# Kernel tuning notes

Measured on AMD Instinct MI355X. Metric: run time of the kernel, lower is better.

The kernel has to match this reference:

```python
import jax, jax.numpy as jnp
import numpy as np

B, T, K, H, HID, OUT = 128, 128, 8, 3, 256, 2
LOG_STD_MIN, LOG_STD_MAX = -20.0, 2.0


def setup_inputs() -> dict:
    key = jax.random.key(0)
    ks = jax.random.split(key, 12)
    def lin(k, fan_in, fan_out, scale=0.05):
        return jax.random.normal(k, (fan_in, fan_out), dtype=jnp.float32) * scale
    return {
        "state": jax.random.normal(ks[0], (B, T, K), dtype=jnp.float32),
        "noise": jax.random.normal(ks[1], (B, T, OUT), dtype=jnp.float32),
        "Wq": lin(ks[2], K, H * K),
        "Wk": lin(ks[3], K, H * K),
        "Wv": lin(ks[4], K, H * K),
        "W1": lin(ks[5], H * K + K, HID),
        "b1": jnp.zeros((HID,), jnp.float32),
        "W2": lin(ks[6], HID, HID),
        "b2": jnp.zeros((HID,), jnp.float32),
        "Wmu": jax.random.uniform(ks[7], (HID, OUT), jnp.float32, -0.003, 0.003),
        "bmu": jax.random.uniform(ks[8], (OUT,), jnp.float32, -0.003, 0.003),
        "Wls": jax.random.uniform(ks[9], (HID, OUT), jnp.float32, -0.003, 0.003),
        "bls": jax.random.uniform(ks[10], (OUT,), jnp.float32, -0.003, 0.003),
    }


def reference(state, noise, Wq, Wk, Wv, W1, b1, W2, b2, Wmu, bmu, Wls, bls):
    b, t, k = state.shape
    h = H
    # off-diagonal gather indices: idx[i, m] = m if m < i else m + 1  (j != i, ascending)
    cols = jnp.arange(t - 1)
    idx = cols[None, :] + (cols[None, :] >= jnp.arange(t)[:, None]).astype(jnp.int32)  # [t, t-1]
    # rel_state[b, i, m] = state[b, idx[i, m]] - state[b, i]   -> [b, t, t-1, k]
    rel = state[:, idx, :] - state[:, :, None, :]
    # per-head projections (no bias)
    q = (state @ Wq).reshape(b, t, h, k)                      # [b, t, h, k]
    keys = (rel @ Wk).reshape(b, t, t - 1, h, k)              # [b, t, t-1, h, k]
    vals = (rel @ Wv).reshape(b, t, t - 1, h, k)
    # each query attends over its own t-1 relative keys
    scores = jnp.einsum("bthk,btmhk->bhtm", q, keys) / jnp.sqrt(jnp.float32(k))
    w = jax.nn.softmax(scores, axis=-1)                       # [b, h, t, t-1]
    x = jnp.einsum("bhtm,btmhk->bthk", w, vals).reshape(b, t, h * k)
    x = jnp.concatenate([x, state], axis=-1)                  # [b, t, h*k + k]
    x = jax.nn.relu(x @ W1 + b1)
    x = jax.nn.relu(x @ W2 + b2)
    mu = jnp.tanh(x @ Wmu + bmu)
    log_std = jnp.tanh(x @ Wls + bls)
    log_std = LOG_STD_MIN + 0.5 * (LOG_STD_MAX - LOG_STD_MIN) * (log_std + 1.0)
    std = jnp.exp(log_std)
    z = mu + std * noise                                      # rsample
    action = jnp.tanh(z)
    half_log_2pi = jnp.float32(0.5 * np.log(2.0 * np.pi))
    normal_lp = -0.5 * noise * noise - log_std - half_log_2pi
    log_prob = normal_lp - jnp.log(1.0 - action * action + 1e-7)
    log_prob = jnp.sum(log_prob, axis=-1, keepdims=True)
    return action, log_prob
```

## Files before the change

kernel.cpp:

```cpp
#include <hip/hip_runtime.h>
#include <math.h>

namespace {
constexpr int B_  = 128;
constexpr int T_  = 128;
constexpr int K_  = 8;
constexpr int H_  = 3;
constexpr int HK_ = 24;
constexpr int HID_ = 256;
constexpr int OUT_ = 2;
}

typedef __attribute__((ext_vector_type(8))) short bf16x8;
typedef __attribute__((ext_vector_type(4))) float f32x4;

__device__ inline unsigned short f2bf(float x) {
    unsigned int u = __float_as_uint(x);
    u += 0x7FFFu + ((u >> 16) & 1u);
    return (unsigned short)(u >> 16);
}
__device__ inline float bflo(unsigned int u) { return __uint_as_float(u << 16); }
__device__ inline float bfhi(unsigned int u) { return __uint_as_float(u & 0xFFFF0000u); }

template <int CTRL>
__device__ inline float dpp_add(float v) {
    int t = __builtin_amdgcn_update_dpp(0, __float_as_int(v), CTRL, 0xF, 0xF, true);
    return v + __int_as_float(t);
}
__device__ inline float red8(float v) {
    v = dpp_add<0xB1>(v);
    v = dpp_add<0x4E>(v);
    return dpp_add<0x141>(v);
}
__device__ inline float red16(float v) {
    return dpp_add<0x140>(red8(v));
}

__global__ __launch_bounds__(256) void prep_kernel(
    const float* __restrict__ W1, const float* __restrict__ W2,
    unsigned short* __restrict__ w1t, unsigned short* __restrict__ w2t)
{
    const int n = threadIdx.x;
    unsigned short tmp[8];
    if (blockIdx.x < 32) {
        const int k0 = blockIdx.x * 8;
        #pragma unroll
        for (int i = 0; i < 8; ++i) tmp[i] = f2bf(W2[(size_t)(k0+i)*HID_ + n]);
        *(bf16x8*)(w2t + (size_t)n*256 + k0) = *(const bf16x8*)tmp;
    } else {
        const int k0 = (blockIdx.x - 32) * 8;
        #pragma unroll
        for (int i = 0; i < 8; ++i) tmp[i] = f2bf(W1[(size_t)(k0+i)*HID_ + n]);
        *(bf16x8*)(w1t + (size_t)n*32 + k0) = *(const bf16x8*)tmp;
    }
}

__global__ __launch_bounds__(256) void fused_actor_kernel(
    const float* __restrict__ state,
    const float* __restrict__ noise,
    const float* __restrict__ Wq, const float* __restrict__ Wk,
    const float* __restrict__ Wv,
    const unsigned short* __restrict__ w1t, const float* __restrict__ b1,
    const unsigned short* __restrict__ w2t, const float* __restrict__ b2,
    const float* __restrict__ Wmu, const float* __restrict__ bmu,
    const float* __restrict__ Wls, const float* __restrict__ bls,
    float* __restrict__ out)
{
    __shared__ float wq_s[K_*HK_], wk_s[K_*HK_], wv_s[K_*HK_];
    __shared__ alignas(16) unsigned short Kb[H_][T_][8];
    __shared__ alignas(16) unsigned short Vb[H_][T_][8];
    __shared__ alignas(16) float Qs[32][HK_];
    __shared__ alignas(16) unsigned short a0b[32][40];
    __shared__ alignas(16) unsigned short x1s[32][264];
    __shared__ alignas(16) float hp[4][32][4];

    const int tid  = threadIdx.x;
    const int b    = blockIdx.x >> 2;
    const int iq   = blockIdx.x & 3;
    const int i0   = iq * 32;
    const int w    = tid >> 6;
    const int lane = tid & 63;
    const float* sb = state + (size_t)b*T_*K_;

    if (tid < K_*HK_) { wq_s[tid]=Wq[tid]; wk_s[tid]=Wk[tid]; wv_s[tid]=Wv[tid]; }
    __syncthreads();

    {
        const int j = tid >> 1, p = tid & 1;
        const float4 s0 = *(const float4*)(sb + j*8);
        const float4 s1 = *(const float4*)(sb + j*8 + 4);
        const float sv[8] = {s0.x,s0.y,s0.z,s0.w,s1.x,s1.y,s1.z,s1.w};
        const float* ws = p ? wv_s : wk_s;
        #pragma unroll
        for (int h = 0; h < H_; ++h) {
            unsigned short pk[8];
            #pragma unroll
            for (int k = 0; k < 8; ++k) {
                const int col = h*8 + k;
                float a = 0.f;
                #pragma unroll
                for (int m = 0; m < K_; ++m) a = fmaf(sv[m], ws[m*HK_+col], a);
                pk[k] = f2bf(a);
            }
            unsigned short* dst = p ? &Vb[h][j][0] : &Kb[h][j][0];
            *(bf16x8*)dst = *(const bf16x8*)pk;
        }
        if (p == 0 && j >= i0 && j < i0 + 32) {
            unsigned short sb16[8];
            #pragma unroll
            for (int k = 0; k < 8; ++k) sb16[k] = f2bf(sv[k]);
            *(bf16x8*)&a0b[j - i0][HK_] = *(const bf16x8*)sb16;
        }
    }
    {
        const int il = tid >> 3;
        const int c0 = (tid & 7) * 3;
        const float4 s0 = *(const float4*)(sb + (i0+il)*8);
        const float4 s1 = *(const float4*)(sb + (i0+il)*8 + 4);
        const float sv[8] = {s0.x,s0.y,s0.z,s0.w,s1.x,s1.y,s1.z,s1.w};
        #pragma unroll
        for (int cc = 0; cc < 3; ++cc) {
            const int col = c0 + cc;
            float aq = 0.f;
            #pragma unroll
            for (int m = 0; m < K_; ++m) aq = fmaf(sv[m], wq_s[m*HK_+col], aq);
            Qs[il][col] = aq * 0.35355339059327373f;
        }
    }
    __syncthreads();

    {
        const int i_sub = lane >> 3, jg = lane & 7;
        #pragma unroll
        for (int p = 0; p < 3; ++p) {
            const int pair = w*3 + p;
            const int h  = pair >> 2;
            const int ig = pair & 3;
            const int il = ig*8 + i_sub;
            const int iglob = i0 + il;
            const float4 q0 = *(const float4*)&Qs[il][h*8];
            const float4 q1 = *(const float4*)&Qs[il][h*8+4];
            float l = 0.f;
            float acc[8] = {0.f,0.f,0.f,0.f,0.f,0.f,0.f,0.f};
            #pragma unroll 4
            for (int t = 0; t < 16; ++t) {
                const int j = t*8 + jg;
                const int4 kk = *(const int4*)&Kb[h][j][0];
                float s;
                s = q0.x * bflo(kk.x) + q0.y * bfhi(kk.x)
                  + q0.z * bflo(kk.y) + q0.w * bfhi(kk.y)
                  + q1.x * bflo(kk.z) + q1.y * bfhi(kk.z)
                  + q1.z * bflo(kk.w) + q1.w * bfhi(kk.w);
                const float e = (j == iglob) ? 0.f : __expf(s);
                l += e;
                const int4 vv = *(const int4*)&Vb[h][j][0];
                acc[0] = fmaf(e, bflo(vv.x), acc[0]);
                acc[1] = fmaf(e, bfhi(vv.x), acc[1]);
                acc[2] = fmaf(e, bflo(vv.y), acc[2]);
                acc[3] = fmaf(e, bfhi(vv.y), acc[3]);
                acc[4] = fmaf(e, bflo(vv.z), acc[4]);
                acc[5] = fmaf(e, bfhi(vv.z), acc[5]);
                acc[6] = fmaf(e, bflo(vv.w), acc[6]);
                acc[7] = fmaf(e, bfhi(vv.w), acc[7]);
            }
            l = red8(l);
            #pragma unroll
            for (int k = 0; k < 8; ++k) acc[k] = red8(acc[k]);
            if (jg == 0) {
                const float rl = 1.f / l;
                const int4 vi = *(const int4*)&Vb[h][iglob][0];
                const float vs[8] = { bflo(vi.x), bfhi(vi.x), bflo(vi.y), bfhi(vi.y),
                                      bflo(vi.z), bfhi(vi.z), bflo(vi.w), bfhi(vi.w) };
                unsigned int r01 = (unsigned int)f2bf(acc[0]*rl - vs[0])
                                 | ((unsigned int)f2bf(acc[1]*rl - vs[1]) << 16);
                unsigned int r23 = (unsigned int)f2bf(acc[2]*rl - vs[2])
                                 | ((unsigned int)f2bf(acc[3]*rl - vs[3]) << 16);
                unsigned int r45 = (unsigned int)f2bf(acc[4]*rl - vs[4])
                                 | ((unsigned int)f2bf(acc[5]*rl - vs[5]) << 16);
                unsigned int r67 = (unsigned int)f2bf(acc[6]*rl - vs[6])
                                 | ((unsigned int)f2bf(acc[7]*rl - vs[7]) << 16);
                int4 rr; rr.x = r01; rr.y = r23; rr.z = r45; rr.w = r67;
                *(int4*)&a0b[il][h*8] = rr;
            }
        }
    }
    __syncthreads();

    const int lq = (tid >> 4) & 3;
    const int ln = tid & 15;

    {
        const bf16x8 a0 = *(const bf16x8*)&a0b[ln][lq*8];
        const bf16x8 a1 = *(const bf16x8*)&a0b[16+ln][lq*8];
        #pragma unroll
        for (int nt = 0; nt < 4; ++nt) {
            const int n0 = (w*4 + nt)*16;
            const bf16x8 bf = *(const bf16x8*)(w1t + (size_t)(n0+ln)*32 + lq*8);
            const float bias = b1[n0+ln];
            f32x4 c = {bias, bias, bias, bias};
            f32x4 d0 = __builtin_amdgcn_mfma_f32_16x16x32_bf16(a0, bf, c, 0, 0, 0);
            f32x4 d1 = __builtin_amdgcn_mfma_f32_16x16x32_bf16(a1, bf, c, 0, 0, 0);
            #pragma unroll
            for (int r = 0; r < 4; ++r) {
                x1s[lq*4 + r][n0+ln]      = f2bf(fmaxf(d0[r], 0.f));
                x1s[16 + lq*4 + r][n0+ln] = f2bf(fmaxf(d1[r], 0.f));
            }
        }
    }
    __syncthreads();

    f32x4 acc2[2][4];
    #pragma unroll
    for (int nt = 0; nt < 4; ++nt) {
        const float bias = b2[(w*4+nt)*16 + ln];
        f32x4 c = {bias, bias, bias, bias};
        acc2[0][nt] = c; acc2[1][nt] = c;
    }
    #pragma unroll 2
    for (int ks = 0; ks < 8; ++ks) {
        const int k0 = ks*32;
        const bf16x8 a0 = *(const bf16x8*)&x1s[ln][k0 + lq*8];
        const bf16x8 a1 = *(const bf16x8*)&x1s[16+ln][k0 + lq*8];
        #pragma unroll
        for (int nt = 0; nt < 4; ++nt) {
            const bf16x8 bf = *(const bf16x8*)(w2t + (size_t)((w*4+nt)*16+ln)*256 + k0 + lq*8);
            acc2[0][nt] = __builtin_amdgcn_mfma_f32_16x16x32_bf16(a0, bf, acc2[0][nt], 0,0,0);
            acc2[1][nt] = __builtin_amdgcn_mfma_f32_16x16x32_bf16(a1, bf, acc2[1][nt], 0,0,0);
        }
    }

    {
        float p[2][4][4];
        #pragma unroll
        for (int mt = 0; mt < 2; ++mt)
            #pragma unroll
            for (int r = 0; r < 4; ++r)
                #pragma unroll
                for (int o = 0; o < 4; ++o) p[mt][r][o] = 0.f;
        #pragma unroll
        for (int nt = 0; nt < 4; ++nt) {
            const int n = (w*4+nt)*16 + ln;
            const float2 wm = *(const float2*)(Wmu + n*OUT_);
            const float2 wl = *(const float2*)(Wls + n*OUT_);
            #pragma unroll
            for (int mt = 0; mt < 2; ++mt) {
                #pragma unroll
                for (int r = 0; r < 4; ++r) {
                    const float x2 = fmaxf(acc2[mt][nt][r], 0.f);
                    p[mt][r][0] = fmaf(x2, wm.x, p[mt][r][0]);
                    p[mt][r][1] = fmaf(x2, wm.y, p[mt][r][1]);
                    p[mt][r][2] = fmaf(x2, wl.x, p[mt][r][2]);
                    p[mt][r][3] = fmaf(x2, wl.y, p[mt][r][3]);
                }
            }
        }
        #pragma unroll
        for (int mt = 0; mt < 2; ++mt)
            #pragma unroll
            for (int r = 0; r < 4; ++r)
                #pragma unroll
                for (int o = 0; o < 4; ++o)
                    p[mt][r][o] = red16(p[mt][r][o]);
        if (ln == 0) {
            #pragma unroll
            for (int mt = 0; mt < 2; ++mt)
                #pragma unroll
                for (int r = 0; r < 4; ++r) {
                    f32x4 pv = {p[mt][r][0], p[mt][r][1], p[mt][r][2], p[mt][r][3]};
                    *(f32x4*)&hp[w][mt*16 + lq*4 + r][0] = pv;
                }
        }
    }
    __syncthreads();

    if (tid < 32) {
        const int r = tid;
        const int grow = b*T_ + i0 + r;
        float pre[4];
        #pragma unroll
        for (int o = 0; o < 4; ++o)
            pre[o] = hp[0][r][o] + hp[1][r][o] + hp[2][r][o] + hp[3][r][o];
        float lp = 0.f;
        #pragma unroll
        for (int o = 0; o < OUT_; ++o) {
            float mu  = tanhf(pre[o]   + bmu[o]);
            float lsp = tanhf(pre[2+o] + bls[o]);
            float log_std = -20.f + 11.f * (lsp + 1.f);
            float sd = __expf(log_std);
            float n  = noise[(size_t)grow*OUT_ + o];
            float z  = fmaf(sd, n, mu);
            float a  = tanhf(z);
            out[(size_t)grow*OUT_ + o] = a;
            lp += -0.5f*n*n - log_std - 0.91893853320467274f
                  - logf(1.f - a*a + 1e-7f);
        }
        out[(size_t)B_*T_*OUT_ + grow] = lp;
    }
}

extern "C" void kernel_launch(void* const* d_in, const int* in_sizes, int n_in,
                              void* d_out, int out_size, void* d_ws, size_t ws_size,
                              hipStream_t stream)
{
    const float* state = (const float*)d_in[0];
    const float* noise = (const float*)d_in[1];
    const float* Wq  = (const float*)d_in[2];
    const float* Wk  = (const float*)d_in[3];
    const float* Wv  = (const float*)d_in[4];
    const float* W1  = (const float*)d_in[5];
    const float* b1  = (const float*)d_in[6];
    const float* W2  = (const float*)d_in[7];
    const float* b2  = (const float*)d_in[8];
    const float* Wmu = (const float*)d_in[9];
    const float* bmu = (const float*)d_in[10];
    const float* Wls = (const float*)d_in[11];
    const float* bls = (const float*)d_in[12];
    float* out = (float*)d_out;

    unsigned short* w1t = (unsigned short*)d_ws;
    unsigned short* w2t = w1t + 8192;

    prep_kernel<<<dim3(36), dim3(256), 0, stream>>>(W1, W2, w1t, w2t);
    fused_actor_kernel<<<dim3(B_*4), dim3(256), 0, stream>>>(
        state, noise, Wq, Wk, Wv, w1t, b1, w2t, b2, Wmu, bmu, Wls, bls, out);
}
```

Before: 101.9 us.

## Compute attention scores and weighted values with MFMA instead of scalar loops

Replaces the per-lane scalar attention loop with bf16 MFMA tiles. QK^T is zero-padded into 16x16x32 MFMAs, and exp weights are written to a shared P buffer unioned with x1s. A second MFMA pass multiplies P by a transposed V layout. Row sums are reduced with DPP and combined across waves through shared memory. This is meant to cut VALU and FMA work in the attention phase. The cost is an extra barrier, quantizing the probabilities to bf16, and wasted MFMA lanes from padding K=8 up to 32.

```diff
diff --git a/kernel.cpp b/kernel.cpp
--- a/kernel.cpp
+++ b/kernel.cpp
@@ -9,6 +9,7 @@
 constexpr int HK_ = 24;
 constexpr int HID_ = 256;
 constexpr int OUT_ = 2;
+constexpr int PBS_ = 144;
 }
 
 typedef __attribute__((ext_vector_type(8))) short bf16x8;
@@ -19,21 +20,18 @@
     u += 0x7FFFu + ((u >> 16) & 1u);
     return (unsigned short)(u >> 16);
 }
-__device__ inline float bflo(unsigned int u) { return __uint_as_float(u << 16); }
-__device__ inline float bfhi(unsigned int u) { return __uint_as_float(u & 0xFFFF0000u); }
+__device__ inline float bf2f(unsigned short v) { return __uint_as_float((unsigned)v << 16); }
 
 template <int CTRL>
 __device__ inline float dpp_add(float v) {
     int t = __builtin_amdgcn_update_dpp(0, __float_as_int(v), CTRL, 0xF, 0xF, true);
     return v + __int_as_float(t);
 }
-__device__ inline float red8(float v) {
+__device__ inline float red16(float v) {
     v = dpp_add<0xB1>(v);
     v = dpp_add<0x4E>(v);
-    return dpp_add<0x141>(v);
-}
-__device__ inline float red16(float v) {
-    return dpp_add<0x140>(red8(v));
+    v = dpp_add<0x141>(v);
+    return dpp_add<0x140>(v);
 }
 
 __global__ __launch_bounds__(256) void prep_kernel(
@@ -67,11 +65,15 @@
     float* __restrict__ out)
 {
     __shared__ float wq_s[K_*HK_], wk_s[K_*HK_], wv_s[K_*HK_];
+    __shared__ alignas(16) unsigned short Qb[32][HK_];
     __shared__ alignas(16) unsigned short Kb[H_][T_][8];
-    __shared__ alignas(16) unsigned short Vb[H_][T_][8];
-    __shared__ alignas(16) float Qs[32][HK_];
+    __shared__ alignas(16) unsigned short Vt[H_][K_][T_];
+    __shared__ alignas(16) float lsum[4][H_][32];
     __shared__ alignas(16) unsigned short a0b[32][40];
-    __shared__ alignas(16) unsigned short x1s[32][264];
+    __shared__ union alignas(16) {
+        unsigned short Pb[H_][32][PBS_];
+        unsigned short x1s[32][264];
+    } u;
     __shared__ alignas(16) float hp[4][32][4];
 
     const int tid  = threadIdx.x;
@@ -79,7 +81,8 @@
     const int iq   = blockIdx.x & 3;
     const int i0   = iq * 32;
     const int w    = tid >> 6;
-    const int lane = tid & 63;
+    const int lq   = (tid >> 4) & 3;
+    const int ln   = tid & 15;
     const float* sb = state + (size_t)b*T_*K_;
 
     if (tid < K_*HK_) { wq_s[tid]=Wq[tid]; wk_s[tid]=Wk[tid]; wv_s[tid]=Wv[tid]; }
@@ -102,8 +105,12 @@
                 for (int m = 0; m < K_; ++m) a = fmaf(sv[m], ws[m*HK_+col], a);
                 pk[k] = f2bf(a);
             }
-            unsigned short* dst = p ? &Vb[h][j][0] : &Kb[h][j][0];
-            *(bf16x8*)dst = *(const bf16x8*)pk;
+            if (p == 0) {
+                *(bf16x8*)&Kb[h][j][0] = *(const bf16x8*)pk;
+            } else {
+                #pragma unroll
+                for (int d = 0; d < 8; ++d) Vt[h][d][j] = pk[d];
+            }
         }
         if (p == 0 && j >= i0 && j < i0 + 32) {
             unsigned short sb16[8];
@@ -124,70 +131,86 @@
             float aq = 0.f;
             #pragma unroll
             for (int m = 0; m < K_; ++m) aq = fmaf(sv[m], wq_s[m*HK_+col], aq);
-            Qs[il][col] = aq * 0.35355339059327373f;
-        }
-    }
-    __syncthreads();
-
-    {
-        const int i_sub = lane >> 3, jg = lane & 7;
-        #pragma unroll
-        for (int p = 0; p < 3; ++p) {
-            const int pair = w*3 + p;
-            const int h  = pair >> 2;
-            const int ig = pair & 3;
-            const int il = ig*8 + i_sub;
-            const int iglob = i0 + il;
-            const float4 q0 = *(const float4*)&Qs[il][h*8];
-            const float4 q1 = *(const float4*)&Qs[il][h*8+4];
-            float l = 0.f;
-            float acc[8] = {0.f,0.f,0.f,0.f,0.f,0.f,0.f,0.f};
-            #pragma unroll 4
-            for (int t = 0; t < 16; ++t) {
-                const int j = t*8 + jg;
-                const int4 kk = *(const int4*)&Kb[h][j][0];
-                float s;
-                s = q0.x * bflo(kk.x) + q0.y * bfhi(kk.x)
-                  + q0.z * bflo(kk.y) + q0.w * bfhi(kk.y)
-                  + q1.x * bflo(kk.z) + q1.y * bfhi(kk.z)
-                  + q1.z * bflo(kk.w) + q1.w * bfhi(kk.w);
-                const float e = (j == iglob) ? 0.f : __expf(s);
-                l += e;
-                const int4 vv = *(const int4*)&Vb[h][j][0];
-                acc[0] = fmaf(e, bflo(vv.x), acc[0]);
-                acc[1] = fmaf(e, bfhi(vv.x), acc[1]);
-                acc[2] = fmaf(e, bflo(vv.y), acc[2]);
-                acc[3] = fmaf(e, bfhi(vv.y), acc[3]);
-                acc[4] = fmaf(e, bflo(vv.z), acc[4]);
-                acc[5] = fmaf(e, bfhi(vv.z), acc[5]);
-                acc[6] = fmaf(e, bflo(vv.w), acc[6]);
-                acc[7] = fmaf(e, bfhi(vv.w), acc[7]);
-            }
-            l = red8(l);
-            #pragma unroll
-            for (int k = 0; k < 8; ++k) acc[k] = red8(acc[k]);
-            if (jg == 0) {
-                const float rl = 1.f / l;
-                const int4 vi = *(const int4*)&Vb[h][iglob][0];
-                const float vs[8] = { bflo(vi.x), bfhi(vi.x), bflo(vi.y), bfhi(vi.y),
-                                      bflo(vi.z), bfhi(vi.z), bflo(vi.w), bfhi(vi.w) };
-                unsigned int r01 = (unsigned int)f2bf(acc[0]*rl - vs[0])
-                                 | ((unsigned int)f2bf(acc[1]*rl - vs[1]) << 16);
-                unsigned int r23 = (unsigned int)f2bf(acc[2]*rl - vs[2])
-                                 | ((unsigned int)f2bf(acc[3]*rl - vs[3]) << 16);
-                unsigned int r45 = (unsigned int)f2bf(acc[4]*rl - vs[4])
-                                 | ((unsigned int)f2bf(acc[5]*rl - vs[5]) << 16);
-                unsigned int r67 = (unsigned int)f2bf(acc[6]*rl - vs[6])
-                                 | ((unsigned int)f2bf(acc[7]*rl - vs[7]) << 16);
-                int4 rr; rr.x = r01; rr.y = r23; rr.z = r45; rr.w = r67;
-                *(int4*)&a0b[il][h*8] = rr;
-            }
-        }
-    }
-    __syncthreads();
-
-    const int lq = (tid >> 4) & 3;
-    const int ln = tid & 15;
+            Qb[il][col] = f2bf(aq * 0.35355339059327373f);
+        }
+    }
+    __syncthreads();
+
+    {
+        const bf16x8 zf = {0,0,0,0,0,0,0,0};
+        const f32x4 c0v = {0.f,0.f,0.f,0.f};
+        float esum[H_][2][4];
+        #pragma unroll
+        for (int h = 0; h < H_; ++h)
+            #pragma unroll
+            for (int mt = 0; mt < 2; ++mt)
+                #pragma unroll
+                for (int r = 0; r < 4; ++r) esum[h][mt][r] = 0.f;
+        #pragma unroll
+        for (int h = 0; h < H_; ++h) {
+            bf16x8 qa[2];
+            #pragma unroll
+            for (int mt = 0; mt < 2; ++mt) {
+                const bf16x8 t = *(const bf16x8*)&Qb[mt*16 + ln][h*8];
+                qa[mt] = (lq == 0) ? t : zf;
+            }
+            #pragma unroll
+            for (int nti = 0; nti < 2; ++nti) {
+                const int nt = w*2 + nti;
+                const bf16x8 tb = *(const bf16x8*)&Kb[h][nt*16 + ln][0];
+                const bf16x8 kf = (lq == 0) ? tb : zf;
+                #pragma unroll
+                for (int mt = 0; mt < 2; ++mt) {
+                    f32x4 s = __builtin_amdgcn_mfma_f32_16x16x32_bf16(qa[mt], kf, c0v, 0,0,0);
+                    #pragma unroll
+                    for (int r = 0; r < 4; ++r) {
+                        const int il = mt*16 + lq*4 + r;
+                        const int j  = nt*16 + ln;
+                        const float e = (j == i0 + il) ? 0.f : __expf(s[r]);
+                        esum[h][mt][r] += e;
+                        u.Pb[h][il][j] = f2bf(e);
+                    }
+                }
+            }
+        }
+        #pragma unroll
+        for (int h = 0; h < H_; ++h)
+            #pragma unroll
+            for (int mt = 0; mt < 2; ++mt)
+                #pragma unroll
+                for (int r = 0; r < 4; ++r) {
+                    const float v = red16(esum[h][mt][r]);
+                    if (ln == 0) lsum[w][h][mt*16 + lq*4 + r] = v;
+                }
+    }
+    __syncthreads();
+
+    {
+        const bf16x8 zf = {0,0,0,0,0,0,0,0};
+        for (int id = w; id < 6; id += 4) {
+            const int h = id >> 1, mt = id & 1;
+            f32x4 x = {0.f,0.f,0.f,0.f};
+            #pragma unroll
+            for (int ks = 0; ks < 4; ++ks) {
+                const int k0 = ks*32;
+                const bf16x8 pa = *(const bf16x8*)&u.Pb[h][mt*16 + ln][k0 + lq*8];
+                const bf16x8 tv = *(const bf16x8*)&Vt[h][ln & 7][k0 + lq*8];
+                const bf16x8 vf = (ln < 8) ? tv : zf;
+                x = __builtin_amdgcn_mfma_f32_16x16x32_bf16(pa, vf, x, 0, 0, 0);
+            }
+            if (ln < 8) {
+                #pragma unroll
+                for (int r = 0; r < 4; ++r) {
+                    const int il = mt*16 + lq*4 + r;
+                    const float l = lsum[0][h][il] + lsum[1][h][il]
+                                  + lsum[2][h][il] + lsum[3][h][il];
+                    const float xatt = x[r] / l - bf2f(Vt[h][ln][i0 + il]);
+                    a0b[il][h*8 + ln] = f2bf(xatt);
+                }
+            }
+        }
+    }
+    __syncthreads();
 
     {
         const bf16x8 a0 = *(const bf16x8*)&a0b[ln][lq*8];
@@ -202,8 +225,8 @@
             f32x4 d1 = __builtin_amdgcn_mfma_f32_16x16x32_bf16(a1, bf, c, 0, 0, 0);
             #pragma unroll
             for (int r = 0; r < 4; ++r) {
-                x1s[lq*4 + r][n0+ln]      = f2bf(fmaxf(d0[r], 0.f));
-                x1s[16 + lq*4 + r][n0+ln] = f2bf(fmaxf(d1[r], 0.f));
+                u.x1s[lq*4 + r][n0+ln]      = f2bf(fmaxf(d0[r], 0.f));
+                u.x1s[16 + lq*4 + r][n0+ln] = f2bf(fmaxf(d1[r], 0.f));
             }
         }
     }
@@ -219,8 +242,8 @@
     #pragma unroll 2
     for (int ks = 0; ks < 8; ++ks) {
         const int k0 = ks*32;
-        const bf16x8 a0 = *(const bf16x8*)&x1s[ln][k0 + lq*8];
-        const bf16x8 a1 = *(const bf16x8*)&x1s[16+ln][k0 + lq*8];
+        const bf16x8 a0 = *(const bf16x8*)&u.x1s[ln][k0 + lq*8];
+        const bf16x8 a1 = *(const bf16x8*)&u.x1s[16+ln][k0 + lq*8];
         #pragma unroll
         for (int nt = 0; nt < 4; ++nt) {
             const bf16x8 bf = *(const bf16x8*)(w2t + (size_t)((w*4+nt)*16+ln)*256 + k0 + lq*8);
```

After: 95.66 us. 1.07x faster.
